# Kernel optimization log

Measured on AMD Instinct MI355X. Metric: run time of the kernel, lower is better.

Reference implementation:

```python
import jax, jax.numpy as jnp
import numpy as np

NEG_INF = -1e10  # matches torch -10000000000.0


def setup_inputs() -> dict:
    key = jax.random.key(0)
    ks = jax.random.split(key, 8)
    L, B, E, H, HID, A = 2048, 32, 512, 512, 512, 512
    input_data = jax.random.normal(ks[0], (L, B, E), dtype=jnp.float32)
    mask = jax.random.randint(ks[1], (L, B), 0, 2, dtype=jnp.int32)
    action_feature = jax.random.normal(ks[2], (B, A), dtype=jnp.float32)
    hidden_state = jax.random.normal(ks[3], (B, H), dtype=jnp.float32)
    state = jax.random.normal(ks[4], (B, H), dtype=jnp.float32)
    W1 = jax.random.normal(ks[5], (H + E, HID), dtype=jnp.float32) * (1.0 / np.sqrt(H + E))
    b1 = jnp.zeros((HID,), dtype=jnp.float32)
    W2 = jax.random.normal(ks[6], (HID, 1), dtype=jnp.float32) * (1.0 / np.sqrt(HID))
    b2 = jnp.zeros((1,), dtype=jnp.float32)
    return {"input_data": input_data, "mask": mask, "action_feature": action_feature,
            "hidden_state": hidden_state, "state": state,
            "W1": W1, "b1": b1, "W2": W2, "b2": b2}


def reference(input_data, mask, action_feature, hidden_state, state, W1, b1, W2, b2):
    # input_data: (L, B, E); hidden_state: (B, H)
    H = hidden_state.shape[-1]
    # query = concat([hidden broadcast over L, input_data], -1); split W1 to avoid
    # materializing the (L, B, H+E) concat.
    W1_h, W1_e = W1[:H], W1[H:]                      # (H, HID), (E, HID)
    pre = hidden_state @ W1_h + b1                   # (B, HID)
    pre = pre[None] + jnp.einsum('lbe,eh->lbh', input_data, W1_e)  # (L, B, HID)
    logit = (jnp.tanh(pre) @ W2).squeeze(-1) + b2[0]  # (L, B)
    logit = jnp.where(mask != 0, logit, NEG_INF)
    p = jax.nn.softmax(logit, axis=0)                 # softmax over L
    ctx = jnp.einsum('lbe,lb->be', input_data, p)     # (B, E)
    return jnp.concatenate([ctx, action_feature], axis=1)
```

## Files before the change

kernel.cpp:

```cpp
#include <hip/hip_runtime.h>
#include <hip/hip_bf16.h>
#include <stdint.h>

#define L_DIM 2048
#define B_DIM 32
#define E_DIM 512
#define HID_DIM 512
#define M_DIM (L_DIM * B_DIM)

typedef float f32x4 __attribute__((ext_vector_type(4)));
typedef short bf16x8 __attribute__((ext_vector_type(8)));

#define OFF_BASE  0
#define OFF_WT    65536
#define OFF_LOGIT 589824
#define OFF_P     851968
#define OFF_PART  1114112

__device__ __forceinline__ unsigned short f2bf(float f) {
  unsigned int u = __float_as_uint(f);
  u = (u + 0x7FFFu + ((u >> 16) & 1u)) >> 16;
  return (unsigned short)u;
}

__device__ __forceinline__ float tanh_fast(float x) {
  float xc = fminf(fmaxf(x, -15.f), 15.f);
  float e = __expf(2.f * xc);
  return (e - 1.f) * __builtin_amdgcn_rcpf(e + 1.f);
}

__device__ __forceinline__ uint4 pack8(const float4& a, const float4& b) {
  uint4 r;
  r.x = (unsigned)f2bf(a.x) | ((unsigned)f2bf(a.y) << 16);
  r.y = (unsigned)f2bf(a.z) | ((unsigned)f2bf(a.w) << 16);
  r.z = (unsigned)f2bf(b.x) | ((unsigned)f2bf(b.y) << 16);
  r.w = (unsigned)f2bf(b.z) | ((unsigned)f2bf(b.w) << 16);
  return r;
}

__global__ __launch_bounds__(256) void k_base(const float* __restrict__ hidden,
                                              const float* __restrict__ W1,
                                              const float* __restrict__ b1,
                                              float* __restrict__ base) {
  const int b = blockIdx.x;
  const int tid = threadIdx.x;
  __shared__ float hs[HID_DIM];
  {
    float2 v = *(const float2*)(hidden + (size_t)b * 512 + tid * 2);
    hs[tid * 2] = v.x; hs[tid * 2 + 1] = v.y;
  }
  __syncthreads();
  const int h = tid * 2;
  float2 b1v = *(const float2*)(b1 + h);
  float ax = b1v.x, ay = b1v.y;
#pragma unroll 8
  for (int e = 0; e < 512; ++e) {
    float2 w = *(const float2*)(W1 + (size_t)e * 512 + h);
    float hv = hs[e];
    ax = fmaf(hv, w.x, ax);
    ay = fmaf(hv, w.y, ay);
  }
  float2 r; r.x = ax; r.y = ay;
  *(float2*)(base + (size_t)b * 512 + h) = r;
}

__global__ __launch_bounds__(256) void k_prep_wt(const float* __restrict__ W1,
                                                 unsigned short* __restrict__ Wt) {
  const int kc = blockIdx.x;
  const int tid = threadIdx.x;
  __shared__ unsigned short sh[32][516];
#pragma unroll
  for (int i = 0; i < 16; ++i) {
    int f4 = i * 256 + tid;
    int r = f4 >> 7;
    int c = (f4 & 127) * 4;
    float4 v = *(const float4*)(W1 + (size_t)(512 + kc * 32 + r) * 512 + c);
    sh[r][c + 0] = f2bf(v.x); sh[r][c + 1] = f2bf(v.y);
    sh[r][c + 2] = f2bf(v.z); sh[r][c + 3] = f2bf(v.w);
  }
  __syncthreads();
#pragma unroll
  for (int i = 0; i < 8; ++i) {
    int u = i * 256 + tid;
    int n = ((u >> 9) << 7) + (((u >> 6) & 7) << 4) + (u & 15);
    int k0 = ((u >> 4) & 3) << 3;
    alignas(16) unsigned short tmp[8];
#pragma unroll
    for (int j = 0; j < 8; ++j) tmp[j] = sh[k0 + j][n];
    *(uint4*)(Wt + ((size_t)kc * 2048 + u) * 8) = *(const uint4*)tmp;
  }
}

__global__ __launch_bounds__(512, 2) void k_logits(
    const float* __restrict__ x, const unsigned short* __restrict__ Wt,
    const float* __restrict__ base, const float* __restrict__ W2,
    float* __restrict__ logit) {
  __shared__ unsigned short xs[2][4096];
  __shared__ unsigned short wl[2][16384];
  const int tid = threadIdx.x;
  const int m0 = blockIdx.x * 128;
  const int wid = tid >> 6, lane = tid & 63;
  const int wm = wid >> 2, wn = wid & 3;
  const int lg = lane >> 4, l15 = lane & 15;

  const int xr = tid >> 2;
  const int xks = tid & 3;
  const float* xsrc = x + (size_t)(m0 + xr) * 512 + xks * 8;
  const int xu = ((xr >> 4) << 6) + (xks << 4) + (xr & 15);

  {
    float4 a0 = *(const float4*)(xsrc + 0);
    float4 a1 = *(const float4*)(xsrc + 4);
    *(uint4*)(&xs[0][xu * 8]) = pack8(a0, a1);
    const uint4* s = (const uint4*)Wt;
#pragma unroll
    for (int j = 0; j < 4; ++j) {
      uint4 w = s[j * 512 + tid];
      *(uint4*)(&wl[0][(j * 512 + tid) * 8]) = w;
    }
  }
  __syncthreads();

  f32x4 acc[4][8];
#pragma unroll
  for (int mi = 0; mi < 4; ++mi)
#pragma unroll
    for (int ni = 0; ni < 8; ++ni) acc[mi][ni] = (f32x4){0.f, 0.f, 0.f, 0.f};

  for (int kc = 0; kc < 16; ++kc) {
    const int cur = kc & 1;
    float4 nxa, nxb; uint4 nw[4];
    if (kc < 15) {
      nxa = *(const float4*)(xsrc + (kc + 1) * 32);
      nxb = *(const float4*)(xsrc + (kc + 1) * 32 + 4);
      const uint4* s = (const uint4*)(Wt) + (size_t)(kc + 1) * 2048;
#pragma unroll
      for (int j = 0; j < 4; ++j) nw[j] = s[j * 512 + tid];
    }
    bf16x8 af[4];
#pragma unroll
    for (int mi = 0; mi < 4; ++mi)
      af[mi] = *(const bf16x8*)(&xs[cur][((wm * 4 + mi) * 64 + lane) * 8]);
    bf16x8 bfv[8];
#pragma unroll
    for (int ni = 0; ni < 8; ++ni)
      bfv[ni] = *(const bf16x8*)(&wl[cur][(wn * 512 + ni * 64 + lane) * 8]);
#pragma unroll
    for (int mi = 0; mi < 4; ++mi)
#pragma unroll
      for (int ni = 0; ni < 8; ++ni)
        acc[mi][ni] = __builtin_amdgcn_mfma_f32_16x16x32_bf16(af[mi], bfv[ni], acc[mi][ni], 0, 0, 0);
    if (kc < 15) {
      const int nb = cur ^ 1;
      *(uint4*)(&xs[nb][xu * 8]) = pack8(nxa, nxb);
#pragma unroll
      for (int j = 0; j < 4; ++j)
        *(uint4*)(&wl[nb][(j * 512 + tid) * 8]) = nw[j];
    }
    __syncthreads();
  }

  float w2v[8];
#pragma unroll
  for (int ni = 0; ni < 8; ++ni) w2v[ni] = W2[wn * 128 + ni * 16 + l15];
  float lsum[4][4];
#pragma unroll
  for (int mi = 0; mi < 4; ++mi) {
#pragma unroll
    for (int rg = 0; rg < 4; ++rg) {
      int m = m0 + wm * 64 + mi * 16 + lg * 4 + rg;
      int bb = m & 31;
      const float* brow = base + (size_t)bb * 512 + wn * 128;
      float s = 0.f;
#pragma unroll
      for (int ni = 0; ni < 8; ++ni) {
        float pre = acc[mi][ni][rg] + brow[ni * 16 + l15];
        s = fmaf(tanh_fast(pre), w2v[ni], s);
      }
      lsum[mi][rg] = s;
    }
  }
  float (*lred)[4][64] = (float (*)[4][64])xs;
#pragma unroll
  for (int mi = 0; mi < 4; ++mi)
#pragma unroll
    for (int rg = 0; rg < 4; ++rg) {
      float v = lsum[mi][rg];
      v += __shfl_xor(v, 1); v += __shfl_xor(v, 2);
      v += __shfl_xor(v, 4); v += __shfl_xor(v, 8);
      if (l15 == 0) lred[wm][wn][mi * 16 + lg * 4 + rg] = v;
    }
  __syncthreads();
  if (tid < 128) {
    const int wmr = tid >> 6, row = tid & 63;
    float v = (lred[wmr][0][row] + lred[wmr][1][row]) +
              (lred[wmr][2][row] + lred[wmr][3][row]);
    logit[m0 + tid] = v;
  }
}

__global__ __launch_bounds__(256) void k_softmax(const float* __restrict__ logit,
                                                 const int* __restrict__ mask,
                                                 float* __restrict__ p) {
  const int b = blockIdx.x, tid = threadIdx.x;
  float lv[8]; float mx = -3.0e38f;
#pragma unroll
  for (int i = 0; i < 8; ++i) {
    int idx = (tid + i * 256) * 32 + b;
    float v = (mask[idx] != 0) ? logit[idx] : -1.0e10f;
    lv[i] = v; mx = fmaxf(mx, v);
  }
  __shared__ float red[8];
  for (int d = 1; d < 64; d <<= 1) mx = fmaxf(mx, __shfl_xor(mx, d));
  if ((tid & 63) == 0) red[tid >> 6] = mx;
  __syncthreads();
  mx = fmaxf(fmaxf(red[0], red[1]), fmaxf(red[2], red[3]));
  float s = 0.f;
#pragma unroll
  for (int i = 0; i < 8; ++i) { lv[i] = __expf(lv[i] - mx); s += lv[i]; }
  for (int d = 1; d < 64; d <<= 1) s += __shfl_xor(s, d);
  __syncthreads();
  if ((tid & 63) == 0) red[4 + (tid >> 6)] = s;
  __syncthreads();
  s = (red[4] + red[5]) + (red[6] + red[7]);
  float inv = 1.f / s;
#pragma unroll
  for (int i = 0; i < 8; ++i) {
    int idx = (tid + i * 256) * 32 + b;
    p[idx] = lv[i] * inv;
  }
}

__global__ __launch_bounds__(128) void k_ctx(const float* __restrict__ x,
                                             const float* __restrict__ p,
                                             float* __restrict__ part) {
  const int blk = blockIdx.x;
  const int b = blk >> 5, ch = blk & 31;
  const int tid = threadIdx.x;
  __shared__ float ps[64];
  const int l0 = ch * 64;
  if (tid < 64) ps[tid] = p[(l0 + tid) * 32 + b];
  __syncthreads();
  const float* xb = x + ((size_t)l0 * 32 + b) * 512 + tid * 4;
  float ax = 0.f, ay = 0.f, az = 0.f, aw = 0.f;
#pragma unroll 4
  for (int i = 0; i < 64; ++i) {
    float4 v = *(const float4*)(xb + (size_t)i * 32 * 512);
    float pv = ps[i];
    ax = fmaf(pv, v.x, ax); ay = fmaf(pv, v.y, ay);
    az = fmaf(pv, v.z, az); aw = fmaf(pv, v.w, aw);
  }
  float4 r; r.x = ax; r.y = ay; r.z = az; r.w = aw;
  *(float4*)(part + (size_t)blk * 512 + tid * 4) = r;
}

__global__ __launch_bounds__(256) void k_final(const float* __restrict__ part,
                                               const float* __restrict__ af,
                                               float* __restrict__ out) {
  const int b = blockIdx.x, tid = threadIdx.x;
  float ax = 0.f, ay = 0.f;
#pragma unroll
  for (int ch = 0; ch < 32; ++ch) {
    float2 v = *(const float2*)(part + ((size_t)(b * 32 + ch) * 512) + tid * 2);
    ax += v.x; ay += v.y;
  }
  float2 r; r.x = ax; r.y = ay;
  *(float2*)(out + (size_t)b * 1024 + tid * 2) = r;
  float2 a = *(const float2*)(af + (size_t)b * 512 + tid * 2);
  *(float2*)(out + (size_t)b * 1024 + 512 + tid * 2) = a;
}

extern "C" void kernel_launch(void* const* d_in, const int* in_sizes, int n_in,
                              void* d_out, int out_size, void* d_ws, size_t ws_size,
                              hipStream_t stream) {
  const float* x      = (const float*)d_in[0];
  const int*   mask   = (const int*)d_in[1];
  const float* af     = (const float*)d_in[2];
  const float* hidden = (const float*)d_in[3];
  const float* W1     = (const float*)d_in[5];
  const float* b1     = (const float*)d_in[6];
  const float* W2     = (const float*)d_in[7];
  float* out = (float*)d_out;
  char* ws = (char*)d_ws;
  float*          base  = (float*)(ws + OFF_BASE);
  unsigned short* Wt    = (unsigned short*)(ws + OFF_WT);
  float*          logit = (float*)(ws + OFF_LOGIT);
  float*          p     = (float*)(ws + OFF_P);
  float*          part  = (float*)(ws + OFF_PART);

  k_base   <<<32,   256, 0, stream>>>(hidden, W1, b1, base);
  k_prep_wt<<<16,   256, 0, stream>>>(W1, Wt);
  k_logits <<<512,  512, 0, stream>>>(x, Wt, base, W2, logit);
  k_softmax<<<32,   256, 0, stream>>>(logit, mask, p);
  k_ctx    <<<1024, 128, 0, stream>>>(x, p, part);
  k_final  <<<32,   256, 0, stream>>>(part, af, out);
}
```

Measured before the change: 118.5 us.

## Shrink logits tile to 64 rows and load W fragments directly from global

```diff
diff --git a/kernel.cpp b/kernel.cpp
--- a/kernel.cpp
+++ b/kernel.cpp
@@ -27,15 +27,6 @@
   float xc = fminf(fmaxf(x, -15.f), 15.f);
   float e = __expf(2.f * xc);
   return (e - 1.f) * __builtin_amdgcn_rcpf(e + 1.f);
-}
-
-__device__ __forceinline__ uint4 pack8(const float4& a, const float4& b) {
-  uint4 r;
-  r.x = (unsigned)f2bf(a.x) | ((unsigned)f2bf(a.y) << 16);
-  r.y = (unsigned)f2bf(a.z) | ((unsigned)f2bf(a.w) << 16);
-  r.z = (unsigned)f2bf(b.x) | ((unsigned)f2bf(b.y) << 16);
-  r.w = (unsigned)f2bf(b.z) | ((unsigned)f2bf(b.w) << 16);
-  return r;
 }
 
 __global__ __launch_bounds__(256) void k_base(const float* __restrict__ hidden,
@@ -91,96 +82,91 @@
   }
 }
 
-__global__ __launch_bounds__(512, 2) void k_logits(
+__global__ __launch_bounds__(512, 4) void k_logits(
     const float* __restrict__ x, const unsigned short* __restrict__ Wt,
     const float* __restrict__ base, const float* __restrict__ W2,
     float* __restrict__ logit) {
-  __shared__ unsigned short xs[2][4096];
-  __shared__ unsigned short wl[2][16384];
-  const int tid = threadIdx.x;
-  const int m0 = blockIdx.x * 128;
-  const int wid = tid >> 6, lane = tid & 63;
-  const int wm = wid >> 2, wn = wid & 3;
+  __shared__ unsigned short xs[2][2048];
+  const int tid = threadIdx.x;
+  const int m0 = blockIdx.x * 64;
+  const int w = tid >> 6, lane = tid & 63;
   const int lg = lane >> 4, l15 = lane & 15;
 
-  const int xr = tid >> 2;
-  const int xks = tid & 3;
-  const float* xsrc = x + (size_t)(m0 + xr) * 512 + xks * 8;
-  const int xu = ((xr >> 4) << 6) + (xks << 4) + (xr & 15);
+  const int row = tid >> 3, seg4 = tid & 7;
+  const int seg8 = seg4 >> 1, half = seg4 & 1;
+  const float* xsrc = x + (size_t)(m0 + row) * 512 + seg4 * 4;
+  const int xsu = ((row >> 4) * 64 + seg8 * 16 + (row & 15)) * 8 + half * 4;
+
+  int ub[4];
+#pragma unroll
+  for (int ni = 0; ni < 4; ++ni) {
+    int nb = w * 64 + ni * 16;
+    ub[ni] = ((nb >> 7) << 9) + (((nb >> 4) & 7) << 6);
+  }
 
   {
-    float4 a0 = *(const float4*)(xsrc + 0);
-    float4 a1 = *(const float4*)(xsrc + 4);
-    *(uint4*)(&xs[0][xu * 8]) = pack8(a0, a1);
-    const uint4* s = (const uint4*)Wt;
-#pragma unroll
-    for (int j = 0; j < 4; ++j) {
-      uint4 w = s[j * 512 + tid];
-      *(uint4*)(&wl[0][(j * 512 + tid) * 8]) = w;
-    }
-  }
-  __syncthreads();
-
-  f32x4 acc[4][8];
+    float4 v = *(const float4*)xsrc;
+    uint2 pk;
+    pk.x = (unsigned)f2bf(v.x) | ((unsigned)f2bf(v.y) << 16);
+    pk.y = (unsigned)f2bf(v.z) | ((unsigned)f2bf(v.w) << 16);
+    *(uint2*)(&xs[0][xsu]) = pk;
+  }
+  __syncthreads();
+
+  f32x4 acc[4][4];
 #pragma unroll
   for (int mi = 0; mi < 4; ++mi)
 #pragma unroll
-    for (int ni = 0; ni < 8; ++ni) acc[mi][ni] = (f32x4){0.f, 0.f, 0.f, 0.f};
+    for (int ni = 0; ni < 4; ++ni) acc[mi][ni] = (f32x4){0.f, 0.f, 0.f, 0.f};
 
   for (int kc = 0; kc < 16; ++kc) {
     const int cur = kc & 1;
-    float4 nxa, nxb; uint4 nw[4];
+    uint4 bw[4];
+    const uint4* bsrc = (const uint4*)Wt + (size_t)kc * 2048;
+#pragma unroll
+    for (int ni = 0; ni < 4; ++ni) bw[ni] = bsrc[ub[ni] + lane];
+    float4 nx;
+    if (kc < 15) nx = *(const float4*)(xsrc + (kc + 1) * 32);
+    bf16x8 af[4];
+#pragma unroll
+    for (int mi = 0; mi < 4; ++mi)
+      af[mi] = *(const bf16x8*)(&xs[cur][(mi * 64 + lane) * 8]);
+#pragma unroll
+    for (int mi = 0; mi < 4; ++mi)
+#pragma unroll
+      for (int ni = 0; ni < 4; ++ni)
+        acc[mi][ni] = __builtin_amdgcn_mfma_f32_16x16x32_bf16(
+            af[mi], *(const bf16x8*)(&bw[ni]), acc[mi][ni], 0, 0, 0);
     if (kc < 15) {
-      nxa = *(const float4*)(xsrc + (kc + 1) * 32);
-      nxb = *(const float4*)(xsrc + (kc + 1) * 32 + 4);
-      const uint4* s = (const uint4*)(Wt) + (size_t)(kc + 1) * 2048;
-#pragma unroll
-      for (int j = 0; j < 4; ++j) nw[j] = s[j * 512 + tid];
-    }
-    bf16x8 af[4];
-#pragma unroll
-    for (int mi = 0; mi < 4; ++mi)
-      af[mi] = *(const bf16x8*)(&xs[cur][((wm * 4 + mi) * 64 + lane) * 8]);
-    bf16x8 bfv[8];
-#pragma unroll
-    for (int ni = 0; ni < 8; ++ni)
-      bfv[ni] = *(const bf16x8*)(&wl[cur][(wn * 512 + ni * 64 + lane) * 8]);
-#pragma unroll
-    for (int mi = 0; mi < 4; ++mi)
-#pragma unroll
-      for (int ni = 0; ni < 8; ++ni)
-        acc[mi][ni] = __builtin_amdgcn_mfma_f32_16x16x32_bf16(af[mi], bfv[ni], acc[mi][ni], 0, 0, 0);
-    if (kc < 15) {
-      const int nb = cur ^ 1;
-      *(uint4*)(&xs[nb][xu * 8]) = pack8(nxa, nxb);
-#pragma unroll
-      for (int j = 0; j < 4; ++j)
-        *(uint4*)(&wl[nb][(j * 512 + tid) * 8]) = nw[j];
+      uint2 pk;
+      pk.x = (unsigned)f2bf(nx.x) | ((unsigned)f2bf(nx.y) << 16);
+      pk.y = (unsigned)f2bf(nx.z) | ((unsigned)f2bf(nx.w) << 16);
+      *(uint2*)(&xs[cur ^ 1][xsu]) = pk;
     }
     __syncthreads();
   }
 
-  float w2v[8];
-#pragma unroll
-  for (int ni = 0; ni < 8; ++ni) w2v[ni] = W2[wn * 128 + ni * 16 + l15];
+  float w2v[4];
+#pragma unroll
+  for (int ni = 0; ni < 4; ++ni) w2v[ni] = W2[w * 64 + ni * 16 + l15];
   float lsum[4][4];
 #pragma unroll
   for (int mi = 0; mi < 4; ++mi) {
 #pragma unroll
     for (int rg = 0; rg < 4; ++rg) {
-      int m = m0 + wm * 64 + mi * 16 + lg * 4 + rg;
+      int m = m0 + mi * 16 + lg * 4 + rg;
       int bb = m & 31;
-      const float* brow = base + (size_t)bb * 512 + wn * 128;
+      const float* brow = base + (size_t)bb * 512 + w * 64;
       float s = 0.f;
 #pragma unroll
-      for (int ni = 0; ni < 8; ++ni) {
+      for (int ni = 0; ni < 4; ++ni) {
         float pre = acc[mi][ni][rg] + brow[ni * 16 + l15];
         s = fmaf(tanh_fast(pre), w2v[ni], s);
       }
       lsum[mi][rg] = s;
     }
   }
-  float (*lred)[4][64] = (float (*)[4][64])xs;
+  float (*lred)[64] = (float (*)[64])xs;
 #pragma unroll
   for (int mi = 0; mi < 4; ++mi)
 #pragma unroll
@@ -188,13 +174,13 @@
       float v = lsum[mi][rg];
       v += __shfl_xor(v, 1); v += __shfl_xor(v, 2);
       v += __shfl_xor(v, 4); v += __shfl_xor(v, 8);
-      if (l15 == 0) lred[wm][wn][mi * 16 + lg * 4 + rg] = v;
+      if (l15 == 0) lred[w][mi * 16 + lg * 4 + rg] = v;
     }
   __syncthreads();
-  if (tid < 128) {
-    const int wmr = tid >> 6, row = tid & 63;
-    float v = (lred[wmr][0][row] + lred[wmr][1][row]) +
-              (lred[wmr][2][row] + lred[wmr][3][row]);
+  if (tid < 64) {
+    float v = 0.f;
+#pragma unroll
+    for (int wq = 0; wq < 8; ++wq) v += lred[wq][tid];
     logit[m0 + tid] = v;
   }
 }
@@ -290,7 +276,7 @@
 
   k_base   <<<32,   256, 0, stream>>>(hidden, W1, b1, base);
   k_prep_wt<<<16,   256, 0, stream>>>(W1, Wt);
-  k_logits <<<512,  512, 0, stream>>>(x, Wt, base, W2, logit);
+  k_logits <<<1024, 512, 0, stream>>>(x, Wt, base, W2, logit);
   k_softmax<<<32,   256, 0, stream>>>(logit, mask, p);
   k_ctx    <<<1024, 128, 0, stream>>>(x, p, part);
   k_final  <<<32,   256, 0, stream>>>(part, af, out);
```

After: 107.3 us. 9.5% less time.
